# Kernel optimization log

Measured on AMD Instinct MI355X. Metric: run time of the kernel, lower is better.

The kernel has to match this reference:

```python
import jax, jax.numpy as jnp
import numpy as np

D_EQUI = 64
D_INV = 256
D_MSG = 64
N_HEADS = 32
D_HEAD = D_INV // N_HEADS
D_FF = 256
D_EDGE_IN = 64
D_EDGE_OUT = 64
D_OUT = D_EQUI + N_HEADS + D_EDGE_OUT  # 160
IN_FEATS = 2 * D_MSG + D_EQUI + D_EDGE_IN  # 256
B, N = 4, 256


def setup_inputs() -> dict:
    key = jax.random.key(0)
    ks = jax.random.split(key, 20)
    s = 0.05
    inp = {
        "equis": jax.random.normal(ks[0], (B, N, 3, D_EQUI), jnp.float32),
        "invs": jax.random.normal(ks[1], (B, N, D_INV), jnp.float32),
        "edges": jax.random.normal(ks[2], (B, N, N, D_EDGE_IN), jnp.float32),
        "adj_matrix": jnp.ones((B, N, N), jnp.int32),
        # _PairwiseMessages params
        "qW": jax.random.normal(ks[3], (D_INV, D_MSG), jnp.float32) * s,
        "qb": jnp.zeros((D_MSG,), jnp.float32),
        "kW": jax.random.normal(ks[4], (D_INV, D_MSG), jnp.float32) * s,
        "kb": jnp.zeros((D_MSG,), jnp.float32),
        "mW1": jax.random.normal(ks[5], (IN_FEATS, D_FF), jnp.float32) * s,
        "mb1": jnp.zeros((D_FF,), jnp.float32),
        "mW2": jax.random.normal(ks[6], (D_FF, D_OUT), jnp.float32) * s,
        "mb2": jnp.zeros((D_OUT,), jnp.float32),
        # _InvAttention params
        "inv_inW": jax.random.normal(ks[7], (D_INV, D_INV), jnp.float32) * s,
        "inv_inb": jnp.zeros((D_INV,), jnp.float32),
        "inv_outW": jax.random.normal(ks[8], (D_INV, D_INV), jnp.float32) * s,
        "inv_outb": jnp.zeros((D_INV,), jnp.float32),
        # _EquiAttention params (no bias)
        "equi_inW": jax.random.normal(ks[9], (D_EQUI, D_EQUI), jnp.float32) * s,
        "equi_outW": jax.random.normal(ks[10], (D_EQUI, D_EQUI), jnp.float32) * s,
    }
    return inp


def _forward(equis, invs, edges, adj_matrix, qW, qb, kW, kb, mW1, mb1, mW2, mb2,
             inv_inW, inv_inb, inv_outW, inv_outb, equi_inW, equi_outW):
    # ---- pairwise messages ----
    # dotprods of equivariant 3-vectors per channel: [B, Nq, Nk, d_equi]
    dot = jnp.einsum("bqdc,bkdc->bqkc", equis, equis)
    qm = invs @ qW + qb  # [B,N,d_msg]
    km = invs @ kW + kb
    Nn = invs.shape[1]
    feats = jnp.concatenate([
        jnp.broadcast_to(qm[:, :, None, :], (qm.shape[0], Nn, Nn, D_MSG)),
        jnp.broadcast_to(km[:, None, :, :], (km.shape[0], Nn, Nn, D_MSG)),
        dot,
        edges,
    ], axis=-1)  # [B,N,N,in_feats]
    msgs = jax.nn.silu(feats @ mW1 + mb1) @ mW2 + mb2  # [B,N,N,d_out]

    # adjacency -> additive mask (0 where connected, -inf otherwise)
    mask = jnp.where(adj_matrix == 0, -jnp.inf, 0.0).astype(msgs.dtype)

    # ---- invariant attention (first n_heads channels) ----
    inv_msgs = msgs[..., :N_HEADS] + mask[..., None]
    attn_i = jax.nn.softmax(inv_msgs, axis=2)  # softmax over kv
    hf = (invs @ inv_inW + inv_inb).reshape(invs.shape[0], Nn, N_HEADS, D_HEAD)
    out_i = jnp.einsum("bqkh,bkhd->bqhd", attn_i, hf)
    w_i = jnp.sqrt(jnp.sum(attn_i * attn_i, axis=2))  # [B,q,H]
    out_i = out_i * w_i[..., None]
    inv_updates = out_i.reshape(invs.shape[0], Nn, D_INV) @ inv_outW + inv_outb

    # ---- equivariant attention (next d_equi channels) ----
    equi_msgs = msgs[..., N_HEADS:N_HEADS + D_EQUI] + mask[..., None]
    attn_e = jax.nn.softmax(equi_msgs, axis=2)  # [B,q,k,c]
    pe = equis @ equi_inW  # [B,N,3,d_equi]
    out_e = jnp.einsum("bqkc,bkdc->bqdc", attn_e, pe)
    w_e = jnp.sqrt(jnp.sum(attn_e * attn_e, axis=2))  # [B,q,c]
    out_e = out_e * w_e[:, :, None, :]
    equi_updates = out_e @ equi_outW  # [B,N,3,d_equi]

    # ---- edge updates (remaining channels) ----
    edge_updates = msgs[..., N_HEADS + D_EQUI:]
    return equi_updates, inv_updates, edge_updates


def reference(equis, invs, edges, adj_matrix, qW, qb, kW, kb, mW1, mb1, mW2, mb2,
              inv_inW, inv_inb, inv_outW, inv_outb, equi_inW, equi_outW):
    return _forward(equis, invs, edges, adj_matrix, qW, qb, kW, kb, mW1, mb1, mW2, mb2,
                    inv_inW, inv_inb, inv_outW, inv_outb, equi_inW, equi_outW)
```

## Files before the change

### kernel.cpp

```cpp
#include <hip/hip_runtime.h>
#include <hip/hip_bf16.h>
#include <math.h>


typedef __attribute__((ext_vector_type(8))) short short8;
typedef __attribute__((ext_vector_type(8))) __bf16 bf16x8;
typedef __attribute__((ext_vector_type(4))) float f32x4;

constexpr int EQUI_OFF = 0;
constexpr int INV_OFF  = 196608;
constexpr int EDGE_OFF = 458752;

__device__ __forceinline__ unsigned short f2bf(float x) {
    unsigned u = __builtin_bit_cast(unsigned, x);
    u = u + 0x7FFFu + ((u >> 16) & 1u);
    return (unsigned short)(u >> 16);
}
__device__ __forceinline__ unsigned pack2(float a, float b) {
    return (unsigned)f2bf(a) | ((unsigned)f2bf(b) << 16);
}
__device__ __forceinline__ float bf2f(unsigned short u) {
    return __builtin_bit_cast(float, ((unsigned)u) << 16);
}
__device__ __forceinline__ f32x4 MFMA(short8 a, short8 b, f32x4 c) {
    return __builtin_amdgcn_mfma_f32_16x16x32_bf16(
        __builtin_bit_cast(bf16x8, a), __builtin_bit_cast(bf16x8, b), c, 0, 0, 0);
}

__global__ void prep_weights(const float* __restrict__ mW1, const float* __restrict__ mW2,
                             short* __restrict__ W1T, short* __restrict__ W2T) {
    int idx = blockIdx.x * 256 + threadIdx.x;
    if (idx < 32768) {
        int n = idx >> 7, kk = idx & 127;
        W1T[idx] = (short)f2bf(mW1[(128 + kk) * 256 + n]);
    } else {
        int i2 = idx - 32768;
        int n = i2 >> 8, f = i2 & 255;
        W2T[i2] = (short)f2bf(mW2[f * 160 + n]);
    }
}

__global__ void prep_proj(const float* __restrict__ invs, const float* __restrict__ equis,
                          const float* __restrict__ qW, const float* __restrict__ qb,
                          const float* __restrict__ kW, const float* __restrict__ kb,
                          const float* __restrict__ inv_inW, const float* __restrict__ inv_inb,
                          const float* __restrict__ equi_inW,
                          float* __restrict__ qm, float* __restrict__ km,
                          float* __restrict__ hf, float* __restrict__ pe) {
    int tid = threadIdx.x;
    if (blockIdx.x < 1024) {
        int r = blockIdx.x;
        __shared__ float sInv[256];
        sInv[tid] = invs[r * 256 + tid];
        __syncthreads();
        if (tid < 64) {
            float acc = qb[tid];
            for (int f = 0; f < 256; ++f) acc += sInv[f] * qW[f * 64 + tid];
            qm[r * 64 + tid] = acc;
        } else if (tid < 128) {
            int c = tid - 64;
            float acc = kb[c];
            for (int f = 0; f < 256; ++f) acc += sInv[f] * kW[f * 64 + c];
            km[r * 64 + c] = acc;
        }
        float acch = inv_inb[tid];
        for (int f = 0; f < 256; ++f) acch += sInv[f] * inv_inW[f * 256 + tid];
        hf[r * 256 + tid] = acch;
    } else {
        int rn = blockIdx.x - 1024;
        if (tid < 192) {
            int d = tid >> 6, c = tid & 63;
            const float* erow = equis + (size_t)rn * 192 + d * 64;
            float acc = 0.f;
            for (int f = 0; f < 64; ++f) acc += erow[f] * equi_inW[f * 64 + c];
            pe[rn * 192 + d * 64 + c] = acc;
        }
    }
}

__global__ void prep_c12(const float* __restrict__ qm, const float* __restrict__ km,
                         const float* __restrict__ mW1, const float* __restrict__ mb1,
                         float* __restrict__ c1, float* __restrict__ c2) {
    int tid = threadIdx.x;
    __shared__ float s[64];
    if (blockIdx.x < 1024) {
        int r = blockIdx.x;
        if (tid < 64) s[tid] = qm[r * 64 + tid];
        __syncthreads();
        float acc = mb1[tid];
        #pragma unroll 8
        for (int k = 0; k < 64; ++k) acc = fmaf(s[k], mW1[k * 256 + tid], acc);
        c1[r * 256 + tid] = acc;
    } else {
        int r = blockIdx.x - 1024;
        if (tid < 64) s[tid] = km[r * 64 + tid];
        __syncthreads();
        float acc = 0.f;
        #pragma unroll 8
        for (int k = 0; k < 64; ++k) acc = fmaf(s[k], mW1[(64 + k) * 256 + tid], acc);
        c2[r * 256 + tid] = acc;
    }
}

__global__ void prep_T(const float* __restrict__ hf, const float* __restrict__ pe,
                       const float* __restrict__ inv_outW, const float* __restrict__ equi_outW,
                       unsigned short* __restrict__ hfT, unsigned short* __restrict__ peT,
                       unsigned short* __restrict__ WoT, unsigned short* __restrict__ EoT) {
    __shared__ float sT[64][65];
    int tid = threadIdx.x, bi = blockIdx.x;
    if (bi < 64) {
        int b = bi >> 4, t = bi & 15, tj = t >> 2, th = t & 3;
        #pragma unroll
        for (int i = 0; i < 16; ++i) { int idx = i * 256 + tid; int jl = idx >> 6, hl = idx & 63;
            sT[jl][hl] = hf[((size_t)(b * 256 + tj * 64 + jl)) * 256 + th * 64 + hl]; }
        __syncthreads();
        #pragma unroll
        for (int i = 0; i < 16; ++i) { int idx = i * 256 + tid; int hl = idx >> 6, jl = idx & 63;
            hfT[((size_t)(b * 256 + th * 64 + hl)) * 256 + tj * 64 + jl] = f2bf(sT[jl][hl]); }
    } else if (bi < 128) {
        int i2 = bi - 64; int b = i2 >> 4, t = i2 & 15, tj = t >> 2, d = t & 3;
        if (d == 3) {
            #pragma unroll
            for (int i = 0; i < 16; ++i) { int idx = i * 256 + tid; int c = idx >> 6, jl = idx & 63;
                peT[((size_t)((b * 64 + c) * 4 + 3)) * 256 + tj * 64 + jl] = 0; }
        } else {
            #pragma unroll
            for (int i = 0; i < 16; ++i) { int idx = i * 256 + tid; int jl = idx >> 6, c = idx & 63;
                sT[jl][c] = pe[((size_t)(b * 256 + tj * 64 + jl)) * 192 + d * 64 + c]; }
            __syncthreads();
            #pragma unroll
            for (int i = 0; i < 16; ++i) { int idx = i * 256 + tid; int c = idx >> 6, jl = idx & 63;
                peT[((size_t)((b * 64 + c) * 4 + d)) * 256 + tj * 64 + jl] = f2bf(sT[jl][c]); }
        }
    } else if (bi < 144) {
        int i2 = bi - 128; int tf = i2 >> 2, tn = i2 & 3;
        #pragma unroll
        for (int i = 0; i < 16; ++i) { int idx = i * 256 + tid; int fl = idx >> 6, nl = idx & 63;
            sT[fl][nl] = inv_outW[(size_t)(tf * 64 + fl) * 256 + tn * 64 + nl]; }
        __syncthreads();
        #pragma unroll
        for (int i = 0; i < 16; ++i) { int idx = i * 256 + tid; int nl = idx >> 6, fl = idx & 63;
            WoT[(size_t)(tn * 64 + nl) * 256 + tf * 64 + fl] = f2bf(sT[fl][nl]); }
    } else {
        #pragma unroll
        for (int i = 0; i < 16; ++i) { int idx = i * 256 + tid; int cl = idx >> 6, c2 = idx & 63;
            sT[cl][c2] = equi_outW[cl * 64 + c2]; }
        __syncthreads();
        #pragma unroll
        for (int i = 0; i < 16; ++i) { int idx = i * 256 + tid; int c2 = idx >> 6, cl = idx & 63;
            EoT[c2 * 64 + cl] = f2bf(sT[cl][c2]); }
    }
}

constexpr int GA_AH = 0;
constexpr int GA_EQ = 32768;
constexpr int GA_MASK = 33536;
constexpr int GA_BYTES = 33792;

__launch_bounds__(256, 4)
__global__ void semla_gemm(const float* __restrict__ equis, const float* __restrict__ edges,
                           const int* __restrict__ adj, const float* __restrict__ mb2,
                           const short* __restrict__ W1T, const short* __restrict__ W2T,
                           const float* __restrict__ c1, const float* __restrict__ c2,
                           float* __restrict__ out, unsigned short* __restrict__ PT) {
    extern __shared__ char smem[];
    float* sEQ   = (float*)(smem + GA_EQ);
    float* sMask = (float*)(smem + GA_MASK);

    const int tid  = threadIdx.x;
    const int lane = tid & 63;
    const int w    = tid >> 6;
    const int bid  = blockIdx.x;
    const int bq   = bid >> 2;
    const int jc   = bid & 3;
    const int b    = bq >> 8;

    const int lrow = lane & 15;
    const int kgrp = (lane >> 4) << 3;
    const int drow = (lane >> 4) << 2;

    if (tid < 192) sEQ[tid] = equis[(size_t)bq * 192 + tid];
    if (tid < 64)  sMask[tid] = adj[(size_t)bq * 256 + (jc << 6) + tid] ? 0.f : -1e30f;

    float c1v[4];
    #pragma unroll
    for (int ni = 0; ni < 4; ++ni)
        c1v[ni] = c1[bq * 256 + (w << 6) + (ni << 4) + lrow];
    const int ntiles = (w < 2) ? 3 : 2;
    const int nbase  = (w < 2) ? w * 48 : 96 + (w - 2) * 32;
    float b2v[3];
    #pragma unroll
    for (int ti = 0; ti < 3; ++ti)
        if (ti < ntiles) b2v[ti] = mb2[nbase + (ti << 4) + lrow];

    auto stA2 = [&](int row, int col, unsigned v) {
        int byte = ((row << 8) + (col << 1)) ^ ((row & 7) << 4);
        *(unsigned*)(smem + GA_AH + byte) = v;
    };
    auto ldA = [&](int row, int kb) -> short8 {
        int byte = ((row << 8) + (kb << 1)) ^ ((row & 7) << 4);
        return *(const short8*)(smem + GA_AH + byte);
    };
    auto stH = [&](int row, int col, unsigned short v) {
        int byte = ((row << 9) + (col << 1)) ^ ((row & 7) << 4);
        *(unsigned short*)(smem + GA_AH + byte) = v;
    };
    auto ldH = [&](int row, int kb) -> short8 {
        int byte = ((row << 9) + (kb << 1)) ^ ((row & 7) << 4);
        return *(const short8*)(smem + GA_AH + byte);
    };

    __syncthreads();

    {
        int r = tid >> 2, qq = tid & 3;
        const float* erow = equis + (size_t)((b << 8) + (jc << 6) + r) * 192;
        #pragma unroll
        for (int i = 0; i < 4; ++i) {
            int c4 = (i << 2) + qq;
            f32x4 a = (f32x4)(0.f);
            #pragma unroll
            for (int d = 0; d < 3; ++d) {
                f32x4 e  = *(const f32x4*)(erow + d * 64 + c4 * 4);
                f32x4 qv = *(const f32x4*)(sEQ + d * 64 + c4 * 4);
                a += e * qv;
            }
            stA2(r, c4 * 4,     pack2(a.x, a.y));
            stA2(r, c4 * 4 + 2, pack2(a.z, a.w));
        }
        const float* ebase = edges + ((size_t)bq * 256 + (jc << 6)) * 64;
        #pragma unroll
        for (int it = 0; it < 4; ++it) {
            int vi = it * 256 + tid;
            f32x4 v = ((const f32x4*)ebase)[vi];
            int rr = vi >> 4, c4 = vi & 15;
            stA2(rr, 64 + c4 * 4,     pack2(v.x, v.y));
            stA2(rr, 64 + c4 * 4 + 2, pack2(v.z, v.w));
        }
    }
    __syncthreads();

    f32x4 acc[4][4];
    #pragma unroll
    for (int mi = 0; mi < 4; ++mi)
        #pragma unroll
        for (int ni = 0; ni < 4; ++ni) acc[mi][ni] = (f32x4)(0.f);

    #pragma unroll
    for (int k0 = 0; k0 < 128; k0 += 32) {
        int kb = k0 + kgrp;
        short8 a0 = ldA(lrow, kb), a1 = ldA(16 + lrow, kb),
               a2 = ldA(32 + lrow, kb), a3 = ldA(48 + lrow, kb);
        short8 bf[4];
        #pragma unroll
        for (int ni = 0; ni < 4; ++ni)
            bf[ni] = *(const short8*)(W1T + ((w << 6) + (ni << 4) + lrow) * 128 + kb);
        #pragma unroll
        for (int ni = 0; ni < 4; ++ni) {
            acc[0][ni] = MFMA(a0, bf[ni], acc[0][ni]);
            acc[1][ni] = MFMA(a1, bf[ni], acc[1][ni]);
            acc[2][ni] = MFMA(a2, bf[ni], acc[2][ni]);
            acc[3][ni] = MFMA(a3, bf[ni], acc[3][ni]);
        }
    }
    __syncthreads();

    const float* c2base = c2 + ((size_t)((b << 8) + (jc << 6)) << 8);
    #pragma unroll
    for (int mi = 0; mi < 4; ++mi)
        #pragma unroll
        for (int r = 0; r < 4; ++r) {
            int row = (mi << 4) + drow + r;
            const float* c2row = c2base + (row << 8);
            #pragma unroll
            for (int ni = 0; ni < 4; ++ni) {
                int n = (w << 6) + (ni << 4) + lrow;
                float x = acc[mi][ni][r] + c1v[ni] + c2row[n];
                float h = x / (1.f + __expf(-x));
                stH(row, n, f2bf(h));
            }
        }
    __syncthreads();

    f32x4 acc2[4][3];
    #pragma unroll
    for (int mi = 0; mi < 4; ++mi)
        #pragma unroll
        for (int ti = 0; ti < 3; ++ti) acc2[mi][ti] = (f32x4)(0.f);

    #pragma unroll
    for (int k0 = 0; k0 < 256; k0 += 32) {
        int kb = k0 + kgrp;
        short8 a0 = ldH(lrow, kb), a1 = ldH(16 + lrow, kb),
               a2 = ldH(32 + lrow, kb), a3 = ldH(48 + lrow, kb);
        short8 bt[3];
        #pragma unroll
        for (int ti = 0; ti < 3; ++ti)
            if (ti < ntiles) bt[ti] = *(const short8*)(W2T + (nbase + (ti << 4) + lrow) * 256 + kb);
        #pragma unroll
        for (int ti = 0; ti < 3; ++ti)
            if (ti < ntiles) {
                acc2[0][ti] = MFMA(a0, bt[ti], acc2[0][ti]);
                acc2[1][ti] = MFMA(a1, bt[ti], acc2[1][ti]);
                acc2[2][ti] = MFMA(a2, bt[ti], acc2[2][ti]);
                acc2[3][ti] = MFMA(a3, bt[ti], acc2[3][ti]);
            }
    }
    __syncthreads();

    if (w < 2) {
        #pragma unroll
        for (int mi = 0; mi < 4; ++mi)
            #pragma unroll
            for (int ti = 0; ti < 3; ++ti) {
                int n = nbase + (ti << 4) + lrow;
                #pragma unroll
                for (int r = 0; r < 4; ++r) {
                    int j = (mi << 4) + drow + r;
                    float v = acc2[mi][ti][r] + b2v[ti] + sMask[j];
                    *(unsigned short*)(smem + n * 136 + j * 2) = f2bf(v);
                }
            }
    } else {
        #pragma unroll
        for (int mi = 0; mi < 4; ++mi)
            #pragma unroll
            for (int ti = 0; ti < 2; ++ti) {
                int n = nbase + (ti << 4) + lrow;
                #pragma unroll
                for (int r = 0; r < 4; ++r) {
                    int j = (jc << 6) + (mi << 4) + drow + r;
                    out[EDGE_OFF + ((size_t)bq * 256 + j) * 64 + (n - 96)] = acc2[mi][ti][r] + b2v[ti];
                }
            }
    }
    __syncthreads();

    if (tid < 192) {
        int n = tid >> 1, half = tid & 1;
        const char* src = smem + n * 136 + half * 64;
        unsigned short* dst = PT + (((size_t)bq * 96 + n) << 8) + (jc << 6) + half * 32;
        #pragma unroll
        for (int i = 0; i < 4; ++i)
            *(short8*)(dst + i * 8) = *(const short8*)(src + i * 16);
    }
}

constexpr int ES_A = 0;
constexpr int ES_W = 32768;
constexpr int ES_BYTES = 33024;

__launch_bounds__(256, 4)
__global__ void semla_einsum(const unsigned short* __restrict__ PT,
                             const unsigned short* __restrict__ hfT,
                             const unsigned short* __restrict__ peT,
                             unsigned short* __restrict__ OIb, unsigned short* __restrict__ OEb) {
    extern __shared__ char smem[];
    float* sW = (float*)(smem + ES_W);
    const int tid = threadIdx.x, lane = tid & 63, w = tid >> 6;
    const int bi = blockIdx.x;
    const int qc = bi & 3;
    const int t  = bi >> 2;
    const int b  = t / 96;
    const int c  = t - 96 * b;
    const int lrow = lane & 15, kgrp = (lane >> 4) << 3, drow = (lane >> 4) << 2;

    #pragma unroll
    for (int i = 0; i < 8; ++i) {
        int id = i * 256 + tid; int row = id >> 5, ck = id & 31;
        size_t src = (((size_t)((b << 8) + (qc << 6) + row) * 96 + c) << 8) + ck * 16;
        short8 v = *(const short8*)(PT + src);
        int byte = ((row << 9) + (ck << 4)) ^ ((row & 7) << 4);
        *(short8*)(smem + ES_A + byte) = v;
    }
    __syncthreads();

    {
        int r = tid >> 2, p = tid & 3;
        float v[64];
        #pragma unroll
        for (int i = 0; i < 8; ++i) {
            int ck = p * 8 + i;
            int byte = ((r << 9) + (ck << 4)) ^ ((r & 7) << 4);
            short8 x = *(const short8*)(smem + ES_A + byte);
            #pragma unroll
            for (int e = 0; e < 8; ++e) v[i * 8 + e] = bf2f((unsigned short)x[e]);
        }
        float m = v[0];
        #pragma unroll
        for (int i = 1; i < 64; ++i) m = fmaxf(m, v[i]);
        m = fmaxf(m, __shfl_xor(m, 1)); m = fmaxf(m, __shfl_xor(m, 2));
        float s = 0.f, q = 0.f;
        #pragma unroll
        for (int i = 0; i < 64; ++i) { float e = __expf(v[i] - m); v[i] = e; s += e; q = fmaf(e, e, q); }
        s += __shfl_xor(s, 1); s += __shfl_xor(s, 2);
        q += __shfl_xor(q, 1); q += __shfl_xor(q, 2);
        float rs = (s > 0.f) ? 1.f / s : 0.f;
        if (p == 0) sW[r] = sqrtf(q) * rs;
        #pragma unroll
        for (int i = 0; i < 8; ++i) {
            int ck = p * 8 + i;
            short8 o;
            #pragma unroll
            for (int e = 0; e < 8; ++e) o[e] = (short)f2bf(v[i * 8 + e] * rs);
            int byte = ((r << 9) + (ck << 4)) ^ ((r & 7) << 4);
            *(short8*)(smem + ES_A + byte) = o;
        }
    }
    __syncthreads();

    const unsigned short* Bbase =
        (c < 32) ? hfT + (((size_t)((b << 8) + (c << 3) + (lrow & 7))) << 8)
                 : peT + (((size_t)((((b << 6) + (c - 32)) << 2) + (lrow & 3))) << 8);
    f32x4 acc = (f32x4)(0.f);
    #pragma unroll
    for (int k0 = 0; k0 < 256; k0 += 32) {
        int kb = k0 + kgrp;
        int byte = ((((w << 4) + lrow) << 9) + (kb << 1)) ^ ((lrow & 7) << 4);
        short8 a = *(const short8*)(smem + ES_A + byte);
        short8 bb = *(const short8*)(Bbase + kb);
        acc = MFMA(a, bb, acc);
    }
    const int nvalid = (c < 32) ? 8 : 3;
    if (lrow < nvalid) {
        #pragma unroll
        for (int r2 = 0; r2 < 4; ++r2) {
            int ql = (w << 4) + drow + r2;
            float val = acc[r2] * sW[ql];
            size_t grow = (size_t)((b << 8) + (qc << 6) + ql);
            if (c < 32) OIb[(grow << 8) + (c << 3) + lrow] = f2bf(val);
            else        OEb[(grow * 3 + lrow) * 64 + (c - 32)] = f2bf(val);
        }
    }
}

constexpr int PJ_BYTES = 32768;

__launch_bounds__(256, 4)
__global__ void semla_proj(const unsigned short* __restrict__ OIb,
                           const unsigned short* __restrict__ OEb,
                           const unsigned short* __restrict__ WoT,
                           const unsigned short* __restrict__ EoT,
                           const float* __restrict__ inv_outb, float* __restrict__ out) {
    extern __shared__ char smem[];
    const int tid = threadIdx.x, lane = tid & 63, w = tid >> 6;
    const int lrow = lane & 15, kgrp = (lane >> 4) << 3, drow = (lane >> 4) << 2;
    const int bi = blockIdx.x;

    if (bi < 32) {
        const int mb = bi >> 1, nb = bi & 1;
        #pragma unroll
        for (int i = 0; i < 8; ++i) {
            int id = i * 256 + tid; int row = id >> 5, ck = id & 31;
            short8 v = *(const short8*)(OIb + (((size_t)(mb * 64 + row)) << 8) + ck * 16);
            int byte = ((row << 9) + (ck << 4)) ^ ((row & 7) << 4);
            *(short8*)(smem + byte) = v;
        }
        __syncthreads();
        f32x4 acc[4][2];
        #pragma unroll
        for (int mi = 0; mi < 4; ++mi)
            #pragma unroll
            for (int ti = 0; ti < 2; ++ti) acc[mi][ti] = (f32x4)(0.f);
        #pragma unroll
        for (int k0 = 0; k0 < 256; k0 += 32) {
            int kb = k0 + kgrp;
            short8 a[4];
            #pragma unroll
            for (int mi = 0; mi < 4; ++mi) {
                int byte = ((((mi << 4) + lrow) << 9) + (kb << 1)) ^ ((lrow & 7) << 4);
                a[mi] = *(const short8*)(smem + byte);
            }
            #pragma unroll
            for (int ti = 0; ti < 2; ++ti) {
                int n = nb * 128 + w * 32 + (ti << 4) + lrow;
                short8 bb = *(const short8*)(WoT + n * 256 + kb);
                #pragma unroll
                for (int mi = 0; mi < 4; ++mi) acc[mi][ti] = MFMA(a[mi], bb, acc[mi][ti]);
            }
        }
        #pragma unroll
        for (int ti = 0; ti < 2; ++ti) {
            int n = nb * 128 + w * 32 + (ti << 4) + lrow;
            float bias = inv_outb[n];
            #pragma unroll
            for (int mi = 0; mi < 4; ++mi)
                #pragma unroll
                for (int r = 0; r < 4; ++r) {
                    int row = mb * 64 + (mi << 4) + drow + r;
                    out[INV_OFF + (size_t)row * 256 + n] = acc[mi][ti][r] + bias;
                }
        }
    } else {
        const int mb = bi - 32;
        #pragma unroll
        for (int i = 0; i < 2; ++i) {
            int id = i * 256 + tid; int row = id >> 3, ck = id & 7;
            short8 v = *(const short8*)(OEb + (((size_t)(mb * 64 + row)) << 6) + ck * 16);
            int byte = ((row << 7) + (ck << 4)) ^ ((row & 7) << 4);
            *(short8*)(smem + byte) = v;
        }
        __syncthreads();
        f32x4 acc[4];
        #pragma unroll
        for (int ni = 0; ni < 4; ++ni) acc[ni] = (f32x4)(0.f);
        #pragma unroll
        for (int k0 = 0; k0 < 64; k0 += 32) {
            int kb = k0 + kgrp;
            int byte = ((((w << 4) + lrow) << 7) + (kb << 1)) ^ ((lrow & 7) << 4);
            short8 a = *(const short8*)(smem + byte);
            #pragma unroll
            for (int ni = 0; ni < 4; ++ni) {
                short8 bb = *(const short8*)(EoT + ((ni << 4) + lrow) * 64 + kb);
                acc[ni] = MFMA(a, bb, acc[ni]);
            }
        }
        #pragma unroll
        for (int ni = 0; ni < 4; ++ni)
            #pragma unroll
            for (int r = 0; r < 4; ++r) {
                int rowg = mb * 64 + (w << 4) + drow + r;
                int bq = rowg / 3, d = rowg - 3 * bq;
                out[EQUI_OFF + (size_t)bq * 192 + d * 64 + (ni << 4) + lrow] = acc[ni][r];
            }
    }
}

extern "C" void kernel_launch(void* const* d_in, const int* in_sizes, int n_in,
                              void* d_out, int out_size, void* d_ws, size_t ws_size,
                              hipStream_t stream) {
    const float* equis    = (const float*)d_in[0];
    const float* invs     = (const float*)d_in[1];
    const float* edges    = (const float*)d_in[2];
    const int*   adj      = (const int*)d_in[3];
    const float* qW       = (const float*)d_in[4];
    const float* qb       = (const float*)d_in[5];
    const float* kW       = (const float*)d_in[6];
    const float* kb       = (const float*)d_in[7];
    const float* mW1      = (const float*)d_in[8];
    const float* mb1      = (const float*)d_in[9];
    const float* mW2      = (const float*)d_in[10];
    const float* mb2      = (const float*)d_in[11];
    const float* inv_inW  = (const float*)d_in[12];
    const float* inv_inb  = (const float*)d_in[13];
    const float* inv_outW = (const float*)d_in[14];
    const float* inv_outb = (const float*)d_in[15];
    const float* equi_inW = (const float*)d_in[16];
    const float* equi_outW= (const float*)d_in[17];

    char* ws = (char*)d_ws;
    short* W1T = (short*)(ws + 0);
    short* W2T = (short*)(ws + 65536);
    float* qm  = (float*)(ws + 147456);
    float* km  = (float*)(ws + 409600);
    float* hf  = (float*)(ws + 671744);
    float* pe  = (float*)(ws + 1720320);
    float* c1  = (float*)(ws + 2506752);
    float* c2  = (float*)(ws + 3555328);
    unsigned short* PT  = (unsigned short*)(ws + 4603904);
    unsigned short* peT = (unsigned short*)(ws + 54935552);
    unsigned short* hfT = (unsigned short*)(ws + 147456);
    unsigned short* OIb = (unsigned short*)(ws + 55459840);
    unsigned short* OEb = (unsigned short*)(ws + 55984128);
    unsigned short* WoT = (unsigned short*)(ws + 56377344);
    unsigned short* EoT = (unsigned short*)(ws + 56508416);

    prep_weights<<<288, 256, 0, stream>>>(mW1, mW2, W1T, W2T);
    prep_proj<<<2048, 256, 0, stream>>>(invs, equis, qW, qb, kW, kb,
                                        inv_inW, inv_inb, equi_inW, qm, km, hf, pe);
    prep_c12<<<2048, 256, 0, stream>>>(qm, km, mW1, mb1, c1, c2);
    prep_T<<<145, 256, 0, stream>>>(hf, pe, inv_outW, equi_outW, hfT, peT, WoT, EoT);
    semla_gemm<<<4096, 256, GA_BYTES, stream>>>(equis, edges, adj, mb2, W1T, W2T,
                                                c1, c2, (float*)d_out, PT);
    semla_einsum<<<1536, 256, ES_BYTES, stream>>>(PT, hfT, peT, OIb, OEb);
    semla_proj<<<80, 256, PJ_BYTES, stream>>>(OIb, OEb, WoT, EoT, inv_outb, (float*)d_out);
}
```

Before: 168.0 us.

## Fold key projection into first MLP GEMM and write PT directly from registers

The separate c2 = km·W1 precompute and its per-element reads in the gemm epilogue are removed. Instead km is appended as 64 extra K columns of the A tile, and the matching W1 rows are added to W1T, so the MFMA loop runs over K=192. The second GEMM for the attention channels is swapped (W2 as A, hidden as B), so results land transposed and go straight to PT without an LDS staging pass and barrier. Float-to-bf16 conversion now uses hardware casts, and SiLU uses rcp. The cost is more MFMA work per block and scattered 2-byte global stores to PT.

```diff
diff --git a/kernel.cpp b/kernel.cpp
--- a/kernel.cpp
+++ b/kernel.cpp
@@ -16,11 +16,16 @@
     u = u + 0x7FFFu + ((u >> 16) & 1u);
     return (unsigned short)(u >> 16);
 }
-__device__ __forceinline__ unsigned pack2(float a, float b) {
-    return (unsigned)f2bf(a) | ((unsigned)f2bf(b) << 16);
-}
 __device__ __forceinline__ float bf2f(unsigned short u) {
     return __builtin_bit_cast(float, ((unsigned)u) << 16);
+}
+__device__ __forceinline__ unsigned short f2bfh(float x) {
+    return __builtin_bit_cast(unsigned short, (__bf16)x);
+}
+__device__ __forceinline__ short8 pk8(f32x4 a, f32x4 b) {
+    bf16x8 r = { (__bf16)a.x, (__bf16)a.y, (__bf16)a.z, (__bf16)a.w,
+                 (__bf16)b.x, (__bf16)b.y, (__bf16)b.z, (__bf16)b.w };
+    return __builtin_bit_cast(short8, r);
 }
 __device__ __forceinline__ f32x4 MFMA(short8 a, short8 b, f32x4 c) {
     return __builtin_amdgcn_mfma_f32_16x16x32_bf16(
@@ -30,11 +35,12 @@
 __global__ void prep_weights(const float* __restrict__ mW1, const float* __restrict__ mW2,
                              short* __restrict__ W1T, short* __restrict__ W2T) {
     int idx = blockIdx.x * 256 + threadIdx.x;
-    if (idx < 32768) {
-        int n = idx >> 7, kk = idx & 127;
-        W1T[idx] = (short)f2bf(mW1[(128 + kk) * 256 + n]);
+    if (idx < 49152) {
+        int n = idx / 192, kk = idx - n * 192;
+        int row = (kk < 128) ? (128 + kk) : (kk - 64);
+        W1T[idx] = (short)f2bf(mW1[row * 256 + n]);
     } else {
-        int i2 = idx - 32768;
+        int i2 = idx - 49152;
         int n = i2 >> 8, f = i2 & 255;
         W2T[i2] = (short)f2bf(mW2[f * 160 + n]);
     }
@@ -78,28 +84,16 @@
     }
 }
 
-__global__ void prep_c12(const float* __restrict__ qm, const float* __restrict__ km,
-                         const float* __restrict__ mW1, const float* __restrict__ mb1,
-                         float* __restrict__ c1, float* __restrict__ c2) {
-    int tid = threadIdx.x;
+__global__ void prep_c1(const float* __restrict__ qm, const float* __restrict__ mW1,
+                        const float* __restrict__ mb1, float* __restrict__ c1) {
+    int tid = threadIdx.x, r = blockIdx.x;
     __shared__ float s[64];
-    if (blockIdx.x < 1024) {
-        int r = blockIdx.x;
-        if (tid < 64) s[tid] = qm[r * 64 + tid];
-        __syncthreads();
-        float acc = mb1[tid];
-        #pragma unroll 8
-        for (int k = 0; k < 64; ++k) acc = fmaf(s[k], mW1[k * 256 + tid], acc);
-        c1[r * 256 + tid] = acc;
-    } else {
-        int r = blockIdx.x - 1024;
-        if (tid < 64) s[tid] = km[r * 64 + tid];
-        __syncthreads();
-        float acc = 0.f;
-        #pragma unroll 8
-        for (int k = 0; k < 64; ++k) acc = fmaf(s[k], mW1[(64 + k) * 256 + tid], acc);
-        c2[r * 256 + tid] = acc;
-    }
+    if (tid < 64) s[tid] = qm[r * 64 + tid];
+    __syncthreads();
+    float acc = mb1[tid];
+    #pragma unroll 8
+    for (int k = 0; k < 64; ++k) acc = fmaf(s[k], mW1[k * 256 + tid], acc);
+    c1[r * 256 + tid] = acc;
 }
 
 __global__ void prep_T(const float* __restrict__ hf, const float* __restrict__ pe,
@@ -152,8 +146,8 @@
     }
 }
 
-constexpr int GA_AH = 0;
-constexpr int GA_EQ = 32768;
+constexpr int GA_AH   = 0;
+constexpr int GA_EQ   = 32768;
 constexpr int GA_MASK = 33536;
 constexpr int GA_BYTES = 33792;
 
@@ -161,7 +155,7 @@
 __global__ void semla_gemm(const float* __restrict__ equis, const float* __restrict__ edges,
                            const int* __restrict__ adj, const float* __restrict__ mb2,
                            const short* __restrict__ W1T, const short* __restrict__ W2T,
-                           const float* __restrict__ c1, const float* __restrict__ c2,
+                           const float* __restrict__ c1, const float* __restrict__ km,
                            float* __restrict__ out, unsigned short* __restrict__ PT) {
     extern __shared__ char smem[];
     float* sEQ   = (float*)(smem + GA_EQ);
@@ -186,19 +180,13 @@
     #pragma unroll
     for (int ni = 0; ni < 4; ++ni)
         c1v[ni] = c1[bq * 256 + (w << 6) + (ni << 4) + lrow];
-    const int ntiles = (w < 2) ? 3 : 2;
-    const int nbase  = (w < 2) ? w * 48 : 96 + (w - 2) * 32;
-    float b2v[3];
-    #pragma unroll
-    for (int ti = 0; ti < 3; ++ti)
-        if (ti < ntiles) b2v[ti] = mb2[nbase + (ti << 4) + lrow];
-
-    auto stA2 = [&](int row, int col, unsigned v) {
-        int byte = ((row << 8) + (col << 1)) ^ ((row & 7) << 4);
-        *(unsigned*)(smem + GA_AH + byte) = v;
+
+    auto stA16 = [&](int row, int colbyte, short8 v) {
+        int byte = (row * 384 + colbyte) ^ ((row & 7) << 4);
+        *(short8*)(smem + GA_AH + byte) = v;
     };
     auto ldA = [&](int row, int kb) -> short8 {
-        int byte = ((row << 8) + (kb << 1)) ^ ((row & 7) << 4);
+        int byte = (row * 384 + (kb << 1)) ^ ((row & 7) << 4);
         return *(const short8*)(smem + GA_AH + byte);
     };
     auto stH = [&](int row, int col, unsigned short v) {
@@ -213,29 +201,34 @@
     __syncthreads();
 
     {
-        int r = tid >> 2, qq = tid & 3;
+        int r = tid >> 2, h = tid & 3;
         const float* erow = equis + (size_t)((b << 8) + (jc << 6) + r) * 192;
         #pragma unroll
-        for (int i = 0; i < 4; ++i) {
-            int c4 = (i << 2) + qq;
-            f32x4 a = (f32x4)(0.f);
+        for (int g = 0; g < 2; ++g) {
+            int cg = h + g * 4;
+            f32x4 lo = (f32x4)(0.f), hi = (f32x4)(0.f);
             #pragma unroll
             for (int d = 0; d < 3; ++d) {
-                f32x4 e  = *(const f32x4*)(erow + d * 64 + c4 * 4);
-                f32x4 qv = *(const f32x4*)(sEQ + d * 64 + c4 * 4);
-                a += e * qv;
-            }
-            stA2(r, c4 * 4,     pack2(a.x, a.y));
-            stA2(r, c4 * 4 + 2, pack2(a.z, a.w));
+                f32x4 e0 = *(const f32x4*)(erow + d * 64 + cg * 8);
+                f32x4 e1 = *(const f32x4*)(erow + d * 64 + cg * 8 + 4);
+                f32x4 q0 = *(const f32x4*)(sEQ + d * 64 + cg * 8);
+                f32x4 q1 = *(const f32x4*)(sEQ + d * 64 + cg * 8 + 4);
+                lo += e0 * q0; hi += e1 * q1;
+            }
+            stA16(r, cg * 16, pk8(lo, hi));
         }
         const float* ebase = edges + ((size_t)bq * 256 + (jc << 6)) * 64;
-        #pragma unroll
-        for (int it = 0; it < 4; ++it) {
-            int vi = it * 256 + tid;
-            f32x4 v = ((const f32x4*)ebase)[vi];
-            int rr = vi >> 4, c4 = vi & 15;
-            stA2(rr, 64 + c4 * 4,     pack2(v.x, v.y));
-            stA2(rr, 64 + c4 * 4 + 2, pack2(v.z, v.w));
+        const float* kbase = km + (size_t)((b << 8) + (jc << 6)) * 64;
+        #pragma unroll
+        for (int it = 0; it < 2; ++it) {
+            int id = it * 256 + tid;
+            int rr = id >> 3, c8 = id & 7;
+            f32x4 e0 = *(const f32x4*)(ebase + rr * 64 + c8 * 8);
+            f32x4 e1 = *(const f32x4*)(ebase + rr * 64 + c8 * 8 + 4);
+            stA16(rr, 128 + c8 * 16, pk8(e0, e1));
+            f32x4 k0 = *(const f32x4*)(kbase + rr * 64 + c8 * 8);
+            f32x4 k1 = *(const f32x4*)(kbase + rr * 64 + c8 * 8 + 4);
+            stA16(rr, 256 + c8 * 16, pk8(k0, k1));
         }
     }
     __syncthreads();
@@ -247,14 +240,14 @@
         for (int ni = 0; ni < 4; ++ni) acc[mi][ni] = (f32x4)(0.f);
 
     #pragma unroll
-    for (int k0 = 0; k0 < 128; k0 += 32) {
+    for (int k0 = 0; k0 < 192; k0 += 32) {
         int kb = k0 + kgrp;
         short8 a0 = ldA(lrow, kb), a1 = ldA(16 + lrow, kb),
                a2 = ldA(32 + lrow, kb), a3 = ldA(48 + lrow, kb);
         short8 bf[4];
         #pragma unroll
         for (int ni = 0; ni < 4; ++ni)
-            bf[ni] = *(const short8*)(W1T + ((w << 6) + (ni << 4) + lrow) * 128 + kb);
+            bf[ni] = *(const short8*)(W1T + ((w << 6) + (ni << 4) + lrow) * 192 + kb);
         #pragma unroll
         for (int ni = 0; ni < 4; ++ni) {
             acc[0][ni] = MFMA(a0, bf[ni], acc[0][ni]);
@@ -265,84 +258,100 @@
     }
     __syncthreads();
 
-    const float* c2base = c2 + ((size_t)((b << 8) + (jc << 6)) << 8);
     #pragma unroll
     for (int mi = 0; mi < 4; ++mi)
         #pragma unroll
         for (int r = 0; r < 4; ++r) {
             int row = (mi << 4) + drow + r;
-            const float* c2row = c2base + (row << 8);
             #pragma unroll
             for (int ni = 0; ni < 4; ++ni) {
                 int n = (w << 6) + (ni << 4) + lrow;
-                float x = acc[mi][ni][r] + c1v[ni] + c2row[n];
-                float h = x / (1.f + __expf(-x));
-                stH(row, n, f2bf(h));
-            }
-        }
-    __syncthreads();
-
-    f32x4 acc2[4][3];
-    #pragma unroll
-    for (int mi = 0; mi < 4; ++mi)
-        #pragma unroll
-        for (int ti = 0; ti < 3; ++ti) acc2[mi][ti] = (f32x4)(0.f);
-
-    #pragma unroll
-    for (int k0 = 0; k0 < 256; k0 += 32) {
-        int kb = k0 + kgrp;
-        short8 a0 = ldH(lrow, kb), a1 = ldH(16 + lrow, kb),
-               a2 = ldH(32 + lrow, kb), a3 = ldH(48 + lrow, kb);
-        short8 bt[3];
-        #pragma unroll
-        for (int ti = 0; ti < 3; ++ti)
-            if (ti < ntiles) bt[ti] = *(const short8*)(W2T + (nbase + (ti << 4) + lrow) * 256 + kb);
-        #pragma unroll
-        for (int ti = 0; ti < 3; ++ti)
-            if (ti < ntiles) {
-                acc2[0][ti] = MFMA(a0, bt[ti], acc2[0][ti]);
-                acc2[1][ti] = MFMA(a1, bt[ti], acc2[1][ti]);
-                acc2[2][ti] = MFMA(a2, bt[ti], acc2[2][ti]);
-                acc2[3][ti] = MFMA(a3, bt[ti], acc2[3][ti]);
-            }
-    }
+                float x = acc[mi][ni][r] + c1v[ni];
+                float hh = x * __builtin_amdgcn_rcpf(1.f + __expf(-x));
+                stH(row, n, f2bfh(hh));
+            }
+        }
     __syncthreads();
 
     if (w < 2) {
-        #pragma unroll
-        for (int mi = 0; mi < 4; ++mi)
-            #pragma unroll
-            for (int ti = 0; ti < 3; ++ti) {
-                int n = nbase + (ti << 4) + lrow;
+        float b2v[3][4];
+        #pragma unroll
+        for (int tn = 0; tn < 3; ++tn)
+            #pragma unroll
+            for (int r = 0; r < 4; ++r)
+                b2v[tn][r] = mb2[w * 48 + tn * 16 + drow + r];
+        float mj[4];
+        #pragma unroll
+        for (int tj = 0; tj < 4; ++tj) mj[tj] = sMask[tj * 16 + lrow];
+
+        f32x4 acc2[3][4];
+        #pragma unroll
+        for (int tn = 0; tn < 3; ++tn)
+            #pragma unroll
+            for (int tj = 0; tj < 4; ++tj) acc2[tn][tj] = (f32x4)(0.f);
+
+        #pragma unroll
+        for (int k0 = 0; k0 < 256; k0 += 32) {
+            int kb = k0 + kgrp;
+            short8 hB[4];
+            #pragma unroll
+            for (int tj = 0; tj < 4; ++tj) hB[tj] = ldH(tj * 16 + lrow, kb);
+            #pragma unroll
+            for (int tn = 0; tn < 3; ++tn) {
+                short8 wA = *(const short8*)(W2T + (w * 48 + tn * 16 + lrow) * 256 + kb);
+                #pragma unroll
+                for (int tj = 0; tj < 4; ++tj)
+                    acc2[tn][tj] = MFMA(wA, hB[tj], acc2[tn][tj]);
+            }
+        }
+        unsigned short* ptbase = PT + (((size_t)bq * 96) << 8) + (jc << 6);
+        #pragma unroll
+        for (int tn = 0; tn < 3; ++tn)
+            #pragma unroll
+            for (int tj = 0; tj < 4; ++tj)
                 #pragma unroll
                 for (int r = 0; r < 4; ++r) {
-                    int j = (mi << 4) + drow + r;
-                    float v = acc2[mi][ti][r] + b2v[ti] + sMask[j];
-                    *(unsigned short*)(smem + n * 136 + j * 2) = f2bf(v);
+                    int n2 = w * 48 + tn * 16 + drow + r;
+                    float v = acc2[tn][tj][r] + b2v[tn][r] + mj[tj];
+                    ptbase[((size_t)n2 << 8) + tj * 16 + lrow] = f2bfh(v);
                 }
-            }
     } else {
+        const int nb = 96 + (w - 2) * 32;
+        float b2v[2];
+        #pragma unroll
+        for (int ti = 0; ti < 2; ++ti) b2v[ti] = mb2[nb + ti * 16 + lrow];
+
+        f32x4 acc2[4][2];
         #pragma unroll
         for (int mi = 0; mi < 4; ++mi)
             #pragma unroll
+            for (int ti = 0; ti < 2; ++ti) acc2[mi][ti] = (f32x4)(0.f);
+
+        #pragma unroll
+        for (int k0 = 0; k0 < 256; k0 += 32) {
+            int kb = k0 + kgrp;
+            short8 a0 = ldH(lrow, kb), a1 = ldH(16 + lrow, kb),
+                   a2 = ldH(32 + lrow, kb), a3 = ldH(48 + lrow, kb);
+            #pragma unroll
             for (int ti = 0; ti < 2; ++ti) {
-                int n = nbase + (ti << 4) + lrow;
+                short8 bb = *(const short8*)(W2T + (nb + ti * 16 + lrow) * 256 + kb);
+                acc2[0][ti] = MFMA(a0, bb, acc2[0][ti]);
+                acc2[1][ti] = MFMA(a1, bb, acc2[1][ti]);
+                acc2[2][ti] = MFMA(a2, bb, acc2[2][ti]);
+                acc2[3][ti] = MFMA(a3, bb, acc2[3][ti]);
+            }
+        }
+        #pragma unroll
+        for (int mi = 0; mi < 4; ++mi)
+            #pragma unroll
+            for (int ti = 0; ti < 2; ++ti) {
+                int n = nb + ti * 16 + lrow;
                 #pragma unroll
                 for (int r = 0; r < 4; ++r) {
                     int j = (jc << 6) + (mi << 4) + drow + r;
                     out[EDGE_OFF + ((size_t)bq * 256 + j) * 64 + (n - 96)] = acc2[mi][ti][r] + b2v[ti];
                 }
             }
-    }
-    __syncthreads();
-
-    if (tid < 192) {
-        int n = tid >> 1, half = tid & 1;
-        const char* src = smem + n * 136 + half * 64;
-        unsigned short* dst = PT + (((size_t)bq * 96 + n) << 8) + (jc << 6) + half * 32;
-        #pragma unroll
-        for (int i = 0; i < 4; ++i)
-            *(short8*)(dst + i * 8) = *(const short8*)(src + i * 16);
     }
 }
 
@@ -402,7 +411,7 @@
             int ck = p * 8 + i;
             short8 o;
             #pragma unroll
-            for (int e = 0; e < 8; ++e) o[e] = (short)f2bf(v[i * 8 + e] * rs);
+            for (int e = 0; e < 8; ++e) o[e] = (short)f2bfh(v[i * 8 + e] * rs);
             int byte = ((r << 9) + (ck << 4)) ^ ((r & 7) << 4);
             *(short8*)(smem + ES_A + byte) = o;
         }
@@ -428,8 +437,8 @@
             int ql = (w << 4) + drow + r2;
             float val = acc[r2] * sW[ql];
             size_t grow = (size_t)((b << 8) + (qc << 6) + ql);
-            if (c < 32) OIb[(grow << 8) + (c << 3) + lrow] = f2bf(val);
-            else        OEb[(grow * 3 + lrow) * 64 + (c - 32)] = f2bf(val);
+            if (c < 32) OIb[(grow << 8) + (c << 3) + lrow] = f2bfh(val);
+            else        OEb[(grow * 3 + lrow) * 64 + (c - 32)] = f2bfh(val);
         }
     }
 }
@@ -550,28 +559,27 @@
 
     char* ws = (char*)d_ws;
     short* W1T = (short*)(ws + 0);
-    short* W2T = (short*)(ws + 65536);
-    float* qm  = (float*)(ws + 147456);
-    float* km  = (float*)(ws + 409600);
-    float* hf  = (float*)(ws + 671744);
-    float* pe  = (float*)(ws + 1720320);
-    float* c1  = (float*)(ws + 2506752);
-    float* c2  = (float*)(ws + 3555328);
-    unsigned short* PT  = (unsigned short*)(ws + 4603904);
-    unsigned short* peT = (unsigned short*)(ws + 54935552);
-    unsigned short* hfT = (unsigned short*)(ws + 147456);
-    unsigned short* OIb = (unsigned short*)(ws + 55459840);
-    unsigned short* OEb = (unsigned short*)(ws + 55984128);
-    unsigned short* WoT = (unsigned short*)(ws + 56377344);
-    unsigned short* EoT = (unsigned short*)(ws + 56508416);
-
-    prep_weights<<<288, 256, 0, stream>>>(mW1, mW2, W1T, W2T);
+    short* W2T = (short*)(ws + 98304);
+    float* qm  = (float*)(ws + 180224);
+    float* km  = (float*)(ws + 442368);
+    float* hf  = (float*)(ws + 704512);
+    float* pe  = (float*)(ws + 1753088);
+    float* c1  = (float*)(ws + 2539520);
+    unsigned short* hfT = (unsigned short*)(ws + 3588096);
+    unsigned short* peT = (unsigned short*)(ws + 4112384);
+    unsigned short* OIb = (unsigned short*)(ws + 4636672);
+    unsigned short* OEb = (unsigned short*)(ws + 5160960);
+    unsigned short* WoT = (unsigned short*)(ws + 5554176);
+    unsigned short* EoT = (unsigned short*)(ws + 5685248);
+    unsigned short* PT  = (unsigned short*)(ws + 5693440);
+
+    prep_weights<<<352, 256, 0, stream>>>(mW1, mW2, W1T, W2T);
     prep_proj<<<2048, 256, 0, stream>>>(invs, equis, qW, qb, kW, kb,
                                         inv_inW, inv_inb, equi_inW, qm, km, hf, pe);
-    prep_c12<<<2048, 256, 0, stream>>>(qm, km, mW1, mb1, c1, c2);
+    prep_c1<<<1024, 256, 0, stream>>>(qm, mW1, mb1, c1);
     prep_T<<<145, 256, 0, stream>>>(hf, pe, inv_outW, equi_outW, hfT, peT, WoT, EoT);
     semla_gemm<<<4096, 256, GA_BYTES, stream>>>(equis, edges, adj, mb2, W1T, W2T,
-                                                c1, c2, (float*)d_out, PT);
+                                                c1, km, (float*)d_out, PT);
     semla_einsum<<<1536, 256, ES_BYTES, stream>>>(PT, hfT, peT, OIb, OEb);
     semla_proj<<<80, 256, PJ_BYTES, stream>>>(OIb, OEb, WoT, EoT, inv_outb, (float*)d_out);
 }
```

Measured after the change: 171.6 us, median of 2. +2.1%, slower.
